# Optimization experiments

Hardware: AMD Instinct MI355X
Metric: run time of the kernel (lower is better)

The kernel has to match this reference:

```python
import jax, jax.numpy as jnp
import numpy as np
from jax import lax

B, T, I, H, O = 64, 128, 512, 256, 512  # input_size = 2*hidden_size (required by module structure)


def setup_inputs() -> dict:
    key = jax.random.key(0)
    ks = jax.random.split(key, 9)
    s = 0.05
    return {
        "input": jax.random.normal(ks[0], (B, T, I), jnp.float32),
        # PyTorch LSTM params, gate order (i, f, g, o); b = b_ih + b_hh folded
        "w_ih_f": jax.random.normal(ks[1], (4 * H, I), jnp.float32) * s,
        "w_hh_f": jax.random.normal(ks[2], (4 * H, H), jnp.float32) * s,
        "b_f": jax.random.normal(ks[3], (4 * H,), jnp.float32) * s,
        "w_ih_b": jax.random.normal(ks[4], (4 * H, I), jnp.float32) * s,
        "w_hh_b": jax.random.normal(ks[5], (4 * H, H), jnp.float32) * s,
        "b_b": jax.random.normal(ks[6], (4 * H,), jnp.float32) * s,
        "W_lin": jax.random.normal(ks[7], (O, 2 * H), jnp.float32) * s,
        "b_lin": jax.random.normal(ks[8], (O,), jnp.float32) * s,
    }


def _lstm_dir(x, w_ih, w_hh, b, reverse=False):
    """Single-direction LSTM over x [B, t, I_in] from zero state -> [B, t, H]."""
    if reverse:
        x = x[:, ::-1]
    bsz = x.shape[0]
    # precompute input projections: [B, t, 4H]
    xp = jnp.einsum('bti,gi->btg', x, w_ih) + b
    h0 = jnp.zeros((bsz, H), x.dtype)
    c0 = jnp.zeros((bsz, H), x.dtype)

    def step(carry, xt):
        h, c = carry
        g = xt + h @ w_hh.T
        i_g, f_g, g_g, o_g = jnp.split(g, 4, axis=-1)
        i_g = jax.nn.sigmoid(i_g)
        f_g = jax.nn.sigmoid(f_g)
        g_g = jnp.tanh(g_g)
        o_g = jax.nn.sigmoid(o_g)
        c = f_g * c + i_g * g_g
        h = o_g * jnp.tanh(c)
        return (h, c), h

    _, hs = lax.scan(step, (h0, c0), jnp.swapaxes(xp, 0, 1))  # [t, B, H]
    hs = jnp.swapaxes(hs, 0, 1)
    if reverse:
        hs = hs[:, ::-1]
    return hs


def reference(input, w_ih_f, w_hh_f, b_f, w_ih_b, w_hh_b, b_b, W_lin, b_lin):
    def bidir(x):
        return jnp.concatenate([
            _lstm_dir(x, w_ih_f, w_hh_f, b_f, reverse=False),
            _lstm_dir(x, w_ih_b, w_hh_b, b_b, reverse=True),
        ], axis=-1)

    # Full-sequence directional runs (causal forward states over a prefix equal the
    # prefix of the full forward run; anticausal backward states over a suffix equal
    # the suffix of the full backward run). Same math as the 50 redundant calls.
    h_fwd_full = _lstm_dir(input, w_ih_f, w_hh_f, b_f, reverse=False)   # [B,T,H]
    h_bwd_full = _lstm_dir(input, w_ih_b, w_hh_b, b_b, reverse=True)    # [B,T,H]

    # rnn(input[:, :i]) for i in 1..25 : forward part is a slice, backward part is fresh
    pre = [jnp.concatenate([h_fwd_full[:, :i],
                            _lstm_dir(input[:, :i], w_ih_b, w_hh_b, b_b, reverse=True)],
                           axis=-1) for i in range(1, 26)]
    # rnn(input[:, j:]) for j in 1..25 : backward part is a slice, forward part is fresh
    suf = [jnp.concatenate([_lstm_dir(input[:, j:], w_ih_f, w_hh_f, b_f, reverse=False),
                            h_bwd_full[:, j:]],
                           axis=-1) for j in range(1, 26)]

    combines = [jnp.concatenate([p, s], axis=1) for p, s in zip(pre, suf)]  # each [B,T,2H]
    combine = jnp.concatenate(combines, axis=2)                             # [B,T,50H]

    # MaxPool2d((1,25), stride (1,25)) over last dim: windows of 25 consecutive channels
    new_input = combine.reshape(combine.shape[0], combine.shape[1], 2 * H, 25).max(axis=-1)

    recurrent = bidir(new_input)                 # [B,T,2H] (input_size == 2H)
    output = recurrent @ W_lin.T + b_lin         # [B,T,O]
    return output
```

## Files before the change

### kernel.cpp

```cpp
#include <hip/hip_runtime.h>
#include <hip/hip_bf16.h>
#include <cstdint>
#include <cstddef>

typedef unsigned short u16;
typedef unsigned int u32;
typedef __attribute__((ext_vector_type(8))) short short8;
typedef __attribute__((ext_vector_type(4))) float f32x4;
typedef __attribute__((ext_vector_type(4))) float f4v;
typedef __attribute__((ext_vector_type(4))) u16 u16x4;

__device__ __forceinline__ u16 f2bf(float f) {
  u32 u = __float_as_uint(f);
  u32 r = (u + 0x7fffu + ((u >> 16) & 1u)) >> 16;
  return (u16)r;
}
__device__ __forceinline__ float bf2f(u16 v) { return __uint_as_float(((u32)v) << 16); }
__device__ __forceinline__ float sigm(float x) { return 1.f / (1.f + __expf(-x)); }
__device__ __forceinline__ float tanh_(float x) {
  x = fminf(fmaxf(x, -30.f), 30.f);
  float e = __expf(-2.f * x);
  return (1.f - e) / (1.f + e);
}

#define SWZ(row, kb) ((kb) ^ (((row) & 7) << 4))

__global__ void cvt_bf16_kernel(const float* __restrict__ src, u16* __restrict__ dst, int n4) {
  int i = blockIdx.x * blockDim.x + threadIdx.x;
  int stride = gridDim.x * blockDim.x;
  for (; i < n4; i += stride) {
    f4v v = *(const f4v*)(src + (size_t)i * 4);
    u16x4 o;
    o.x = f2bf(v.x); o.y = f2bf(v.y); o.z = f2bf(v.z); o.w = f2bf(v.w);
    *(u16x4*)(dst + (size_t)i * 4) = o;
  }
}

__global__ void split_input_kernel(const float* __restrict__ src, u16* __restrict__ dst, int total) {
  int idx = blockIdx.x * blockDim.x + threadIdx.x;
  int stride = gridDim.x * blockDim.x;
  for (; idx < total; idx += stride) {
    int r = idx >> 9, c = idx & 511;
    float x = src[idx];
    u16 hi = f2bf(x);
    u16 lo = f2bf(x - bf2f(hi));
    u16* d = dst + (size_t)r * 1536;
    d[c] = hi; d[512 + c] = lo; d[1024 + c] = hi;
  }
}
__global__ void split_w_kernel(const float* __restrict__ src, u16* __restrict__ dst) {
  int idx = blockIdx.x * blockDim.x + threadIdx.x;
  int r = idx >> 9, c = idx & 511;
  float x = src[idx];
  u16 hi = f2bf(x);
  u16 lo = f2bf(x - bf2f(hi));
  u16* d = dst + (size_t)r * 1536;
  d[c] = hi; d[512 + c] = hi; d[1024 + c] = lo;
}

__global__ void fill_u32_kernel(u32* __restrict__ p, u32 val, int n) {
  int i = blockIdx.x * blockDim.x + threadIdx.x;
  int stride = gridDim.x * blockDim.x;
  for (; i < n; i += stride) p[i] = val;
}

__global__ __launch_bounds__(256, 1) void gemm_bt_kernel(
    const u16* __restrict__ A, int lda, const u16* __restrict__ W, int ldw,
    const float* __restrict__ b0, const float* __restrict__ b1,
    float* __restrict__ C0, float* __restrict__ C1, int nsplit,
    int M, int K) {
  __shared__ __align__(16) u16 As[128 * 64];
  __shared__ __align__(16) u16 Bs[128 * 64];
  const int m0 = blockIdx.y * 128, n0 = blockIdx.x * 128;
  const int tid = threadIdx.x;
  const int w = tid >> 6, l = tid & 63;
  const int wr = w >> 1, wc = w & 1;
  const int lhi = l >> 4, llo = l & 15;

  f32x4 acc[4][4];
#pragma unroll
  for (int a = 0; a < 4; ++a)
#pragma unroll
    for (int b = 0; b < 4; ++b) acc[a][b] = (f32x4){0.f, 0.f, 0.f, 0.f};

  for (int k0 = 0; k0 < K; k0 += 64) {
    __syncthreads();
#pragma unroll
    for (int it = 0; it < 4; ++it) {
      int off = it * 4096 + tid * 16;
      int row = off >> 7, kb = off & 127;
      short8 va = *(const short8*)((const char*)A + ((size_t)(m0 + row) * lda + k0) * 2 + kb);
      *(short8*)((char*)As + row * 128 + SWZ(row, kb)) = va;
      short8 vb = *(const short8*)((const char*)W + ((size_t)(n0 + row) * ldw + k0) * 2 + kb);
      *(short8*)((char*)Bs + row * 128 + SWZ(row, kb)) = vb;
    }
    __syncthreads();
    short8 af[4][2], bf[4][2];
#pragma unroll
    for (int mt = 0; mt < 4; ++mt)
#pragma unroll
      for (int ks = 0; ks < 2; ++ks) {
        int row = wr * 64 + mt * 16 + llo;
        int kb = ks * 64 + lhi * 16;
        af[mt][ks] = *(const short8*)((const char*)As + row * 128 + SWZ(row, kb));
      }
#pragma unroll
    for (int nt = 0; nt < 4; ++nt)
#pragma unroll
      for (int ks = 0; ks < 2; ++ks) {
        int row = wc * 64 + nt * 16 + llo;
        int kb = ks * 64 + lhi * 16;
        bf[nt][ks] = *(const short8*)((const char*)Bs + row * 128 + SWZ(row, kb));
      }
#pragma unroll
    for (int ks = 0; ks < 2; ++ks)
#pragma unroll
      for (int mt = 0; mt < 4; ++mt)
#pragma unroll
        for (int nt = 0; nt < 4; ++nt)
          acc[mt][nt] = __builtin_amdgcn_mfma_f32_16x16x32_bf16(af[mt][ks], bf[nt][ks], acc[mt][nt], 0, 0, 0);
  }
#pragma unroll
  for (int mt = 0; mt < 4; ++mt)
#pragma unroll
    for (int nt = 0; nt < 4; ++nt) {
      int col = n0 + wc * 64 + nt * 16 + llo;
      const float* bp; float* Cp; int cc;
      if (col < nsplit) { bp = b0; Cp = C0; cc = col; }
      else              { bp = b1; Cp = C1; cc = col - nsplit; }
      float bz = bp[cc];
#pragma unroll
      for (int i = 0; i < 4; ++i) {
        int row = m0 + wr * 64 + mt * 16 + lhi * 4 + i;
        Cp[(size_t)row * nsplit + cc] = acc[mt][nt][i] + bz;
      }
    }
}

__global__ __launch_bounds__(512, 1) void scan_kernel(
    const u16* __restrict__ Wf, const u16* __restrict__ Wb,
    const float* __restrict__ xpF, const float* __restrict__ xpB,
    u16* __restrict__ outF, u16* __restrict__ outB,
    u16* __restrict__ pA, u16* __restrict__ pB, int phase) {
  __shared__ __align__(16) u16 hlds[16 * 256];
  const int bid = blockIdx.x;
  const int nb = (phase == 1) ? 104 : 4;
  const bool fwd = bid < nb;
  const int id = fwd ? bid : bid - nb;
  const int run = (phase == 1) ? (id >> 2) : 0;
  const int q4 = (phase == 1) ? (id & 3) : id;
  const int qbase = q4 * 16;
  const u16* W = fwd ? Wf : Wb;
  const float* xp = fwd ? xpF : xpB;
  u16* out = fwd ? outF : outB;
  const int ostride = (phase == 1) ? 256 : 512;
  const bool store_out = (phase == 2) || (run == 0);
  const int flatbase = store_out ? 0 : ((run - 1) * 512 + (fwd ? 0 : 256));
  const int qlo = (flatbase * 5243) >> 17;
  const int qhi = ((flatbase + 255) * 5243) >> 17;
  int t0, tstep, nsteps;
  if (fwd) {
    t0 = (phase == 1) ? run : 0; tstep = 1; nsteps = 128 - t0;
  } else {
    int s = (phase == 1) ? (run == 0 ? 127 : run - 1) : 127;
    t0 = s; tstep = -1; nsteps = s + 1;
  }
  const int tid = threadIdx.x;
  const int w = tid >> 6, l = tid & 63;
  const int lhi = l >> 4, llo = l & 15;
  const int wrow = tid / 12, wq = tid - wrow * 12;

  for (int i = tid; i < 16 * 256; i += 512) hlds[i] = 0;
  float cst[8];
#pragma unroll
  for (int i = 0; i < 8; ++i) cst[i] = 0.f;
  __syncthreads();

  const char* Wl = (const char*)W + (size_t)(w * 32 + llo) * 512 + lhi * 16;

  int t = t0, tprev = t0;
  for (int it = 0; it < nsteps; ++it, t += tstep) {
    f32x4 acc[8];
    {
      const float* xpl = xp + ((size_t)(qbase + lhi * 4) * 128 + t) * 1024 + w * 32 + llo;
#pragma unroll
      for (int tt = 0; tt < 8; ++tt) {
        int nofs = (tt >> 1) * 256 + (tt & 1) * 16;
#pragma unroll
        for (int i = 0; i < 4; ++i)
          acc[tt][i] = xpl[(size_t)i * 131072 + nofs];
      }
    }
    short8 af[8];
#pragma unroll
    for (int ks = 0; ks < 8; ++ks) {
      int kb = ks * 64 + lhi * 16;
      af[ks] = *(const short8*)((const char*)hlds + llo * 512 + SWZ(llo, kb));
    }
    if (!store_out && it > 0 && tid < 192) {
      int q = qlo + wq;
      if (q <= qhi) {
        int lo = q * 25 - flatbase;
        int chlo = lo < 0 ? 0 : lo;
        int chhi = (lo + 24) > 255 ? 255 : (lo + 24);
        float m = -3.4e38f;
        for (int ch = chlo; ch <= chhi; ++ch)
          m = fmaxf(m, bf2f(*(const u16*)((const char*)hlds + ((wrow * 512 + ch * 2) ^ ((wrow & 7) << 4)))));
        u16* dst = (lo < 0) ? pB : pA;
        dst[(size_t)((qbase + wrow) * 128 + tprev) * 512 + q] = f2bf(m);
      }
    }
    short8 bufA[8], bufB[8];
#pragma unroll
    for (int ks = 0; ks < 8; ++ks)
      bufA[ks] = *(const short8*)(Wl + (size_t)ks * 64);
#pragma unroll
    for (int ks = 0; ks < 8; ++ks)
      bufB[ks] = *(const short8*)(Wl + (size_t)16 * 512 + ks * 64);
#pragma unroll
    for (int tt = 0; tt < 8; ++tt) {
      int nb2 = ((tt + 2) >> 1) * 256 + ((tt + 2) & 1) * 16;
#pragma unroll
      for (int ks = 0; ks < 8; ++ks) {
        if (tt & 1) {
          acc[tt] = __builtin_amdgcn_mfma_f32_16x16x32_bf16(af[ks], bufB[ks], acc[tt], 0, 0, 0);
          if (tt < 6) bufB[ks] = *(const short8*)(Wl + (size_t)nb2 * 512 + ks * 64);
        } else {
          acc[tt] = __builtin_amdgcn_mfma_f32_16x16x32_bf16(af[ks], bufA[ks], acc[tt], 0, 0, 0);
          if (tt < 6) bufA[ks] = *(const short8*)(Wl + (size_t)nb2 * 512 + ks * 64);
        }
      }
    }
    float hv[8];
#pragma unroll
    for (int hf = 0; hf < 2; ++hf)
#pragma unroll
      for (int i = 0; i < 4; ++i) {
        float ig = sigm(acc[0 + hf][i]);
        float fg = sigm(acc[2 + hf][i]);
        float gg = tanh_(acc[4 + hf][i]);
        float og = sigm(acc[6 + hf][i]);
        float c = fg * cst[hf * 4 + i] + ig * gg;
        cst[hf * 4 + i] = c;
        hv[hf * 4 + i] = og * tanh_(c);
      }
    __syncthreads();
#pragma unroll
    for (int hf = 0; hf < 2; ++hf)
#pragma unroll
      for (int i = 0; i < 4; ++i) {
        int row = lhi * 4 + i;
        int ch = w * 32 + hf * 16 + llo;
        u16 hb = f2bf(hv[hf * 4 + i]);
        *(u16*)((char*)hlds + ((row * 512 + ch * 2) ^ ((row & 7) << 4))) = hb;
        if (store_out)
          out[((size_t)(qbase + row) * 128 + t) * ostride + ch] = hb;
      }
    __syncthreads();
    tprev = t;
  }
  if (!store_out && tid < 192) {
    int q = qlo + wq;
    if (q <= qhi) {
      int lo = q * 25 - flatbase;
      int chlo = lo < 0 ? 0 : lo;
      int chhi = (lo + 24) > 255 ? 255 : (lo + 24);
      float m = -3.4e38f;
      for (int ch = chlo; ch <= chhi; ++ch)
        m = fmaxf(m, bf2f(*(const u16*)((const char*)hlds + ((wrow * 512 + ch * 2) ^ ((wrow & 7) << 4)))));
      u16* dst = (lo < 0) ? pB : pA;
      dst[(size_t)((qbase + wrow) * 128 + tprev) * 512 + q] = f2bf(m);
    }
  }
}

__global__ void finish_kernel(const u16* __restrict__ pA, const u16* __restrict__ pB,
                              const u16* __restrict__ HFfull, const u16* __restrict__ HBfull,
                              u16* __restrict__ NI) {
  const int bt = blockIdx.x;
  const int t = bt & 127;
  const int qidx = threadIdx.x;
  float m = fmaxf(bf2f(pA[(size_t)bt * 512 + qidx]), bf2f(pB[(size_t)bt * 512 + qidx]));
  const int base = qidx * 25;
#pragma unroll
  for (int r = 0; r < 25; ++r) {
    int idx = base + r;
    int k = idx >> 9;
    int c = idx & 511;
    if (c < 256) {
      if (t <= k) m = fmaxf(m, bf2f(HFfull[(size_t)bt * 256 + c]));
    } else {
      if (t > k) m = fmaxf(m, bf2f(HBfull[(size_t)bt * 256 + (c - 256)]));
    }
  }
  NI[(size_t)bt * 512 + qidx] = f2bf(m);
}

extern "C" void kernel_launch(void* const* d_in, const int* in_sizes, int n_in,
                              void* d_out, int out_size, void* d_ws, size_t ws_size,
                              hipStream_t stream) {
  (void)in_sizes; (void)n_in; (void)out_size; (void)ws_size;
  const float* input  = (const float*)d_in[0];
  const float* w_ih_f = (const float*)d_in[1];
  const float* w_hh_f = (const float*)d_in[2];
  const float* b_f    = (const float*)d_in[3];
  const float* w_ih_b = (const float*)d_in[4];
  const float* w_hh_b = (const float*)d_in[5];
  const float* b_b    = (const float*)d_in[6];
  const float* W_lin  = (const float*)d_in[7];
  const float* b_lin  = (const float*)d_in[8];

  char* ws = (char*)d_ws;
  size_t off = 0;
  auto alloc = [&](size_t bytes) {
    char* p = ws + off;
    off = (off + bytes + 255) & ~(size_t)255;
    return p;
  };
  u16* WIH2  = (u16*)alloc(6291456);
  u16* WHHF  = (u16*)alloc(524288);
  u16* WHHB  = (u16*)alloc(524288);
  u16* WLIN  = (u16*)alloc(524288);
  float* XPF = (float*)alloc(33554432);
  float* XPB = (float*)alloc(33554432);
  u16* NIbf  = (u16*)alloc(8388608);
  u16* HFfull = (u16*)alloc(4194304);
  u16* HBfull = (u16*)alloc(4194304);
  u16* XH    = (u16*)alloc(25165824);
  u16* pA    = XH;
  u16* pB    = XH + 4194304;
  u16* REC   = HFfull;

  split_input_kernel<<<dim3(4096), dim3(256), 0, stream>>>(input, XH, 4194304);
  split_w_kernel<<<dim3(2048), dim3(256), 0, stream>>>(w_ih_f, WIH2);
  split_w_kernel<<<dim3(2048), dim3(256), 0, stream>>>(w_ih_b, WIH2 + (size_t)1024 * 1536);
  cvt_bf16_kernel<<<dim3(256), dim3(256), 0, stream>>>(w_hh_f, WHHF, 65536);
  cvt_bf16_kernel<<<dim3(256), dim3(256), 0, stream>>>(w_hh_b, WHHB, 65536);
  cvt_bf16_kernel<<<dim3(256), dim3(256), 0, stream>>>(W_lin, WLIN, 65536);

  gemm_bt_kernel<<<dim3(16, 64), dim3(256), 0, stream>>>(XH, 1536, WIH2, 1536,
      b_f, b_b, XPF, XPB, 1024, 8192, 1536);

  fill_u32_kernel<<<dim3(2048), dim3(256), 0, stream>>>((u32*)pA, 0xFF80FF80u, 4194304);

  scan_kernel<<<dim3(208), dim3(512), 0, stream>>>(WHHF, WHHB, XPF, XPB, HFfull, HBfull, pA, pB, 1);

  finish_kernel<<<dim3(8192), dim3(512), 0, stream>>>(pA, pB, HFfull, HBfull, NIbf);

  gemm_bt_kernel<<<dim3(16, 64), dim3(256), 0, stream>>>(NIbf, 512, WIH2, 1536,
      b_f, b_b, XPF, XPB, 1024, 8192, 512);

  scan_kernel<<<dim3(8), dim3(512), 0, stream>>>(WHHF, WHHB, XPF, XPB, REC, REC + 256, pA, pB, 2);

  gemm_bt_kernel<<<dim3(4, 64), dim3(256), 0, stream>>>(REC, 512, WLIN, 512,
      b_lin, b_lin, (float*)d_out, (float*)d_out, 512, 8192, 512);
}
```

Before: 3.319 ms.

## Batch 16 scan runs per block with masking and double-buffered hidden state

Phase 1 of the scan kernel now packs 16 runs of 4 batch rows into one 64-row MFMA tile per block, 64 blocks instead of 208 blocks of 16 rows each. Each recurrent weight fragment loaded from global memory is reused across four M-tiles, and runs that have not started are masked so their state stays zero. The hidden state is double-buffered in LDS, which removes one barrier per step, and the weight and h fragments are software-pipelined across the K loop. In exchange, masked runs waste MFMA work, only 64 CUs are used, and each block now loops over the longest run's step count.

```diff
diff --git a/kernel.cpp b/kernel.cpp
--- a/kernel.cpp
+++ b/kernel.cpp
@@ -137,139 +137,198 @@
     }
 }
 
+template<int NSLOT, int NR, int PHASE>
 __global__ __launch_bounds__(512, 1) void scan_kernel(
     const u16* __restrict__ Wf, const u16* __restrict__ Wb,
     const float* __restrict__ xpF, const float* __restrict__ xpB,
     u16* __restrict__ outF, u16* __restrict__ outB,
-    u16* __restrict__ pA, u16* __restrict__ pB, int phase) {
-  __shared__ __align__(16) u16 hlds[16 * 256];
+    u16* __restrict__ pA, u16* __restrict__ pB) {
+  constexpr int MT = (NSLOT * NR) / 16;
+  constexpr int NV = NSLOT * NR;
+  __shared__ __align__(16) u16 hlds[2][NV * 256];
+
   const int bid = blockIdx.x;
-  const int nb = (phase == 1) ? 104 : 4;
-  const bool fwd = bid < nb;
-  const int id = fwd ? bid : bid - nb;
-  const int run = (phase == 1) ? (id >> 2) : 0;
-  const int q4 = (phase == 1) ? (id & 3) : id;
-  const int qbase = q4 * 16;
+  int dir, grp, rgbase;
+  if (PHASE == 1) { dir = bid >> 5; grp = (bid >> 4) & 1; rgbase = (bid & 15) * NR; }
+  else            { dir = bid >> 2; grp = 0;              rgbase = (bid & 3) * NR; }
+  const bool fwd = (dir == 0);
   const u16* W = fwd ? Wf : Wb;
   const float* xp = fwd ? xpF : xpB;
   u16* out = fwd ? outF : outB;
-  const int ostride = (phase == 1) ? 256 : 512;
-  const bool store_out = (phase == 2) || (run == 0);
-  const int flatbase = store_out ? 0 : ((run - 1) * 512 + (fwd ? 0 : 256));
-  const int qlo = (flatbase * 5243) >> 17;
-  const int qhi = ((flatbase + 255) * 5243) >> 17;
-  int t0, tstep, nsteps;
-  if (fwd) {
-    t0 = (phase == 1) ? run : 0; tstep = 1; nsteps = 128 - t0;
+  const int runbase = grp * 16;
+
+  int t0, nsteps, tstep;
+  if (PHASE == 2) {
+    tstep = fwd ? 1 : -1; t0 = fwd ? 0 : 127; nsteps = 128;
+  } else if (fwd) {
+    tstep = 1;  if (grp == 0) { t0 = 0;   nsteps = 128; } else { t0 = 16; nsteps = 112; }
   } else {
-    int s = (phase == 1) ? (run == 0 ? 127 : run - 1) : 127;
-    t0 = s; tstep = -1; nsteps = s + 1;
-  }
+    tstep = -1; if (grp == 0) { t0 = 127; nsteps = 128; } else { t0 = 24; nsteps = 25;  }
+  }
+
   const int tid = threadIdx.x;
   const int w = tid >> 6, l = tid & 63;
   const int lhi = l >> 4, llo = l & 15;
-  const int wrow = tid / 12, wq = tid - wrow * 12;
-
-  for (int i = tid; i < 16 * 256; i += 512) hlds[i] = 0;
-  float cst[8];
-#pragma unroll
-  for (int i = 0; i < 8; ++i) cst[i] = 0.f;
+
+  for (int i = tid; i < NV * 256; i += 512) { hlds[0][i] = 0; hlds[1][i] = 0; }
+  float cst[2][MT][4];
+#pragma unroll
+  for (int p = 0; p < 2; ++p)
+#pragma unroll
+    for (int mt = 0; mt < MT; ++mt)
+#pragma unroll
+      for (int i = 0; i < 4; ++i) cst[p][mt][i] = 0.f;
   __syncthreads();
 
-  const char* Wl = (const char*)W + (size_t)(w * 32 + llo) * 512 + lhi * 16;
-
+  const char* Wl = (const char*)W + (size_t)(w * 16 + llo) * 512 + lhi * 16;
+
+  int cur = 0;
   int t = t0, tprev = t0;
   for (int it = 0; it < nsteps; ++it, t += tstep) {
-    f32x4 acc[8];
-    {
-      const float* xpl = xp + ((size_t)(qbase + lhi * 4) * 128 + t) * 1024 + w * 32 + llo;
-#pragma unroll
-      for (int tt = 0; tt < 8; ++tt) {
-        int nofs = (tt >> 1) * 256 + (tt & 1) * 16;
-#pragma unroll
-        for (int i = 0; i < 4; ++i)
-          acc[tt][i] = xpl[(size_t)i * 131072 + nofs];
-      }
-    }
-    short8 af[8];
-#pragma unroll
-    for (int ks = 0; ks < 8; ++ks) {
-      int kb = ks * 64 + lhi * 16;
-      af[ks] = *(const short8*)((const char*)hlds + llo * 512 + SWZ(llo, kb));
-    }
-    if (!store_out && it > 0 && tid < 192) {
-      int q = qlo + wq;
-      if (q <= qhi) {
-        int lo = q * 25 - flatbase;
-        int chlo = lo < 0 ? 0 : lo;
-        int chhi = (lo + 24) > 255 ? 255 : (lo + 24);
-        float m = -3.4e38f;
-        for (int ch = chlo; ch <= chhi; ++ch)
-          m = fmaxf(m, bf2f(*(const u16*)((const char*)hlds + ((wrow * 512 + ch * 2) ^ ((wrow & 7) << 4)))));
-        u16* dst = (lo < 0) ? pB : pA;
-        dst[(size_t)((qbase + wrow) * 128 + tprev) * 512 + q] = f2bf(m);
-      }
-    }
-    short8 bufA[8], bufB[8];
-#pragma unroll
-    for (int ks = 0; ks < 8; ++ks)
-      bufA[ks] = *(const short8*)(Wl + (size_t)ks * 64);
-#pragma unroll
-    for (int ks = 0; ks < 8; ++ks)
-      bufB[ks] = *(const short8*)(Wl + (size_t)16 * 512 + ks * 64);
-#pragma unroll
-    for (int tt = 0; tt < 8; ++tt) {
-      int nb2 = ((tt + 2) >> 1) * 256 + ((tt + 2) & 1) * 16;
+    const u16* hb = hlds[cur];
+    u16* hw = hlds[cur ^ 1];
+
+    if (PHASE == 1 && it > 0) {
+#pragma unroll
+      for (int rep = 0; rep < 2; ++rep) {
+        int jj = tid + rep * 512;
+        if (jj < 768) {
+          int slot = jj / 48, rem = jj - slot * 48;
+          int row = rem / 12, ws = rem - row * 12;
+          int j = runbase + slot;
+          if (j >= 1 && j <= 25 && (fwd ? (tprev >= j) : (tprev <= j - 1))) {
+            int flatbase = (j - 1) * 512 + (fwd ? 0 : 256);
+            int qlo = (flatbase * 5243) >> 17;
+            int qhi = ((flatbase + 255) * 5243) >> 17;
+            int q = qlo + ws;
+            if (q <= qhi) {
+              int lo = q * 25 - flatbase;
+              int chlo = lo < 0 ? 0 : lo, chhi = lo + 24 > 255 ? 255 : lo + 24;
+              int vrow = slot * NR + row;
+              float m = -3.4e38f;
+              for (int ch = chlo; ch <= chhi; ++ch)
+                m = fmaxf(m, bf2f(*(const u16*)((const char*)hb + ((vrow * 512 + ch * 2) ^ ((vrow & 7) << 4)))));
+              u16* dst = (lo < 0) ? pB : pA;
+              dst[((size_t)(rgbase + row) * 128 + tprev) * 512 + q] = f2bf(m);
+            }
+          }
+        }
+      }
+    }
+
+#pragma unroll
+    for (int p = 0; p < 2; ++p) {
+      float xq[4][4];
+#pragma unroll
+      for (int g = 0; g < 4; ++g)
+#pragma unroll
+        for (int i = 0; i < 4; ++i) {
+          int brow = (NR == 4) ? i : (lhi * 4 + i);
+          xq[g][i] = xp[((size_t)(rgbase + brow) * 128 + t) * 1024 + g * 256 + p * 128 + w * 16 + llo];
+        }
+
+      f32x4 acc[MT][4];
+#pragma unroll
+      for (int mt = 0; mt < MT; ++mt)
+#pragma unroll
+        for (int g = 0; g < 4; ++g) acc[mt][g] = (f32x4){0.f, 0.f, 0.f, 0.f};
+
+      short8 Wb3[3][4];
+      short8 afb[2][MT];
+#pragma unroll
+      for (int g = 0; g < 4; ++g) {
+        size_t go = (size_t)(g * 256 + p * 128) * 512;
+        Wb3[0][g] = *(const short8*)(Wl + go);
+        Wb3[1][g] = *(const short8*)(Wl + go + 64);
+      }
+#pragma unroll
+      for (int mt = 0; mt < MT; ++mt) {
+        int vrow = mt * 16 + llo;
+        afb[0][mt] = *(const short8*)((const char*)hb + vrow * 512 + SWZ(vrow, lhi * 16));
+      }
 #pragma unroll
       for (int ks = 0; ks < 8; ++ks) {
-        if (tt & 1) {
-          acc[tt] = __builtin_amdgcn_mfma_f32_16x16x32_bf16(af[ks], bufB[ks], acc[tt], 0, 0, 0);
-          if (tt < 6) bufB[ks] = *(const short8*)(Wl + (size_t)nb2 * 512 + ks * 64);
-        } else {
-          acc[tt] = __builtin_amdgcn_mfma_f32_16x16x32_bf16(af[ks], bufA[ks], acc[tt], 0, 0, 0);
-          if (tt < 6) bufA[ks] = *(const short8*)(Wl + (size_t)nb2 * 512 + ks * 64);
-        }
-      }
-    }
-    float hv[8];
-#pragma unroll
-    for (int hf = 0; hf < 2; ++hf)
-#pragma unroll
-      for (int i = 0; i < 4; ++i) {
-        float ig = sigm(acc[0 + hf][i]);
-        float fg = sigm(acc[2 + hf][i]);
-        float gg = tanh_(acc[4 + hf][i]);
-        float og = sigm(acc[6 + hf][i]);
-        float c = fg * cst[hf * 4 + i] + ig * gg;
-        cst[hf * 4 + i] = c;
-        hv[hf * 4 + i] = og * tanh_(c);
-      }
+        if (ks < 6) {
+#pragma unroll
+          for (int g = 0; g < 4; ++g) {
+            size_t go = (size_t)(g * 256 + p * 128) * 512;
+            Wb3[(ks + 2) % 3][g] = *(const short8*)(Wl + go + (ks + 2) * 64);
+          }
+        }
+        if (ks < 7) {
+#pragma unroll
+          for (int mt = 0; mt < MT; ++mt) {
+            int vrow = mt * 16 + llo;
+            afb[(ks + 1) & 1][mt] = *(const short8*)((const char*)hb + vrow * 512 + SWZ(vrow, (ks + 1) * 64 + lhi * 16));
+          }
+        }
+#pragma unroll
+        for (int g = 0; g < 4; ++g)
+#pragma unroll
+          for (int mt = 0; mt < MT; ++mt)
+            acc[mt][g] = __builtin_amdgcn_mfma_f32_16x16x32_bf16(afb[ks & 1][mt], Wb3[ks % 3][g], acc[mt][g], 0, 0, 0);
+      }
+
+#pragma unroll
+      for (int mt = 0; mt < MT; ++mt)
+#pragma unroll
+        for (int i = 0; i < 4; ++i) {
+          int vrow = mt * 16 + lhi * 4 + i;
+          int run = runbase + vrow / NR;
+          bool act;
+          if (PHASE == 2) act = true;
+          else if (fwd)   act = (run <= 25) && (t >= run);
+          else            act = (run == 0) || ((run <= 25) && (t <= run - 1));
+          float ig = sigm(acc[mt][0][i] + xq[0][i]);
+          float fg = sigm(acc[mt][1][i] + xq[1][i]);
+          float gg = tanh_(acc[mt][2][i] + xq[2][i]);
+          float og = sigm(acc[mt][3][i] + xq[3][i]);
+          float c = fg * cst[p][mt][i] + ig * gg;
+          c = act ? c : 0.f;
+          cst[p][mt][i] = c;
+          float h = act ? og * tanh_(c) : 0.f;
+          u16 hbv = f2bf(h);
+          int ch = p * 128 + w * 16 + llo;
+          *(u16*)((char*)hw + ((vrow * 512 + ch * 2) ^ ((vrow & 7) << 4))) = hbv;
+          if (PHASE == 2) {
+            out[((size_t)(rgbase + vrow) * 128 + t) * 512 + ch] = hbv;
+          } else if (grp == 0 && mt == 0 && lhi == 0) {
+            out[((size_t)(rgbase + i) * 128 + t) * 256 + ch] = hbv;
+          }
+        }
+    }
+
     __syncthreads();
-#pragma unroll
-    for (int hf = 0; hf < 2; ++hf)
-#pragma unroll
-      for (int i = 0; i < 4; ++i) {
-        int row = lhi * 4 + i;
-        int ch = w * 32 + hf * 16 + llo;
-        u16 hb = f2bf(hv[hf * 4 + i]);
-        *(u16*)((char*)hlds + ((row * 512 + ch * 2) ^ ((row & 7) << 4))) = hb;
-        if (store_out)
-          out[((size_t)(qbase + row) * 128 + t) * ostride + ch] = hb;
-      }
-    __syncthreads();
+    cur ^= 1;
     tprev = t;
   }
-  if (!store_out && tid < 192) {
-    int q = qlo + wq;
-    if (q <= qhi) {
-      int lo = q * 25 - flatbase;
-      int chlo = lo < 0 ? 0 : lo;
-      int chhi = (lo + 24) > 255 ? 255 : (lo + 24);
-      float m = -3.4e38f;
-      for (int ch = chlo; ch <= chhi; ++ch)
-        m = fmaxf(m, bf2f(*(const u16*)((const char*)hlds + ((wrow * 512 + ch * 2) ^ ((wrow & 7) << 4)))));
-      u16* dst = (lo < 0) ? pB : pA;
-      dst[(size_t)((qbase + wrow) * 128 + tprev) * 512 + q] = f2bf(m);
+
+  if (PHASE == 1) {
+    const u16* hb = hlds[cur];
+#pragma unroll
+    for (int rep = 0; rep < 2; ++rep) {
+      int jj = tid + rep * 512;
+      if (jj < 768) {
+        int slot = jj / 48, rem = jj - slot * 48;
+        int row = rem / 12, ws = rem - row * 12;
+        int j = runbase + slot;
+        if (j >= 1 && j <= 25 && (fwd ? (tprev >= j) : (tprev <= j - 1))) {
+          int flatbase = (j - 1) * 512 + (fwd ? 0 : 256);
+          int qlo = (flatbase * 5243) >> 17;
+          int qhi = ((flatbase + 255) * 5243) >> 17;
+          int q = qlo + ws;
+          if (q <= qhi) {
+            int lo = q * 25 - flatbase;
+            int chlo = lo < 0 ? 0 : lo, chhi = lo + 24 > 255 ? 255 : lo + 24;
+            int vrow = slot * NR + row;
+            float m = -3.4e38f;
+            for (int ch = chlo; ch <= chhi; ++ch)
+              m = fmaxf(m, bf2f(*(const u16*)((const char*)hb + ((vrow * 512 + ch * 2) ^ ((vrow & 7) << 4)))));
+            u16* dst = (lo < 0) ? pB : pA;
+            dst[((size_t)(rgbase + row) * 128 + tprev) * 512 + q] = f2bf(m);
+          }
+        }
+      }
     }
   }
 }
@@ -343,14 +402,16 @@
 
   fill_u32_kernel<<<dim3(2048), dim3(256), 0, stream>>>((u32*)pA, 0xFF80FF80u, 4194304);
 
-  scan_kernel<<<dim3(208), dim3(512), 0, stream>>>(WHHF, WHHB, XPF, XPB, HFfull, HBfull, pA, pB, 1);
+  scan_kernel<16, 4, 1><<<dim3(64), dim3(512), 0, stream>>>(WHHF, WHHB, XPF, XPB,
+      HFfull, HBfull, pA, pB);
 
   finish_kernel<<<dim3(8192), dim3(512), 0, stream>>>(pA, pB, HFfull, HBfull, NIbf);
 
   gemm_bt_kernel<<<dim3(16, 64), dim3(256), 0, stream>>>(NIbf, 512, WIH2, 1536,
       b_f, b_b, XPF, XPB, 1024, 8192, 512);
 
-  scan_kernel<<<dim3(8), dim3(512), 0, stream>>>(WHHF, WHHB, XPF, XPB, REC, REC + 256, pA, pB, 2);
+  scan_kernel<1, 16, 2><<<dim3(8), dim3(512), 0, stream>>>(WHHF, WHHB, XPF, XPB,
+      REC, REC + 256, pA, pB);
 
   gemm_bt_kernel<<<dim3(4, 64), dim3(256), 0, stream>>>(REC, 512, WLIN, 512,
       b_lin, b_lin, (float*)d_out, (float*)d_out, 512, 8192, 512);
```

Measured after the change: 5.368 ms. +61.7%, slower.
